# Performance work log

Measured on AMD Instinct MI355X. Metric: run time of the kernel, lower is better.

## Reference

```python
import jax, jax.numpy as jnp
import numpy as np

BINS = 6  # torch.histc(bins=6, min=0, max=256) in rarity()


def _border_mask(h, w, dtype):
    m = jnp.ones((h, w), dtype)
    return m.at[0, :].set(0).at[-1, :].set(0).at[:, 0].set(0).at[:, -1].set(0)


def _norm(x, lo, hi, axes):
    # normalize_tensor: map to [lo,hi]; all-zeros if constant map
    mn = x.min(axes, keepdims=True)
    mx = x.max(axes, keepdims=True)
    d = mx - mn
    ds = jnp.where(d == 0, jnp.ones_like(d), d)
    out = (x - mn) / ds * (hi - lo) + lo
    return jnp.where(d == 0, jnp.zeros_like(out), out)


def _ponder(x, axes):
    # map_ponderation: normalize to [0,1] then scale by (max-mean)^2
    w = (x.max(axes, keepdims=True) - x.mean(axes, keepdims=True)) ** 2
    return _norm(x, 0.0, 1.0, axes) * w


def _rarity_all(ch):
    # Vectorized rarity() over all channels. ch: [C,H,W]
    C, H, W = ch.shape
    ch = ch * _border_mask(H, W, ch.dtype)          # zero 1-px border
    ch = _norm(ch, 0.0, 256.0, (1, 2))              # per-channel -> [0,256]
    # torch.histc over [0,256]: bin = floor(v*bins/256), max value in last bin
    bin_idx = jnp.clip((ch * (BINS / 256.0)).astype(jnp.int32), 0, BINS - 1)
    hist = jax.nn.one_hot(bin_idx, BINS, dtype=ch.dtype).sum((1, 2))  # [C,BINS]
    hist = hist / hist.sum(-1, keepdims=True)
    hist = -jnp.log(hist + 1e-4)
    # lookup: (channel*bins - 1).long().clamp(0, bins-1)  (channel in [0,256], as in source)
    lut_idx = jnp.clip((ch * BINS - 1).astype(jnp.int32), 0, BINS - 1)
    dst = hist[jnp.arange(C)[:, None, None], lut_idx]  # [C,H,W] rarity lookup
    dst = _norm(dst, 0.0, 1.0, (1, 2))
    return _ponder(dst, (1, 2))


def _apply_rarity(x):
    # x: [1,C,H,W] -> [H,W]
    ch = x[0]
    H, W = ch.shape[-2:]
    r = _rarity_all(ch)
    # channel 0: ponderated again, no extra border zeroing (as in source)
    p0 = _ponder(r[0], (0, 1))
    rest = r[1:] * _border_mask(H, W, r.dtype)  # channels 1..C-1: border zeroed
    p = p0 + _ponder(rest, (1, 2)).sum(0)
    return _norm(p, 0.0, 1.0, (0, 1))  # threshold=None -> no thresholding


def _resize240(m):
    # T.Resize((240,240), bilinear) ~ half-pixel linear resize
    return jax.image.resize(m, (240, 240), method='linear')


def _forward(layers):
    # group layers into packs by spatial resolution (static, shapes known)
    packs = {}
    for t in layers:
        packs.setdefault(t.shape[-2:], []).append(t)
    group_maps = []
    for pack in packs.values():
        maps = [_resize240(_apply_rarity(t)) for t in pack]
        fused = maps[0] * 0.0
        for m in maps:  # fuse_itti
            fused = fused + _ponder(m, (0, 1))
        group_maps.append(_norm(fused, 0.0, 256.0, (0, 1)))
    groups = jnp.stack(group_maps, -1)  # [240,240,n_packs]
    return groups.sum(-1), groups


def setup_inputs() -> dict:
    key = jax.random.key(0)
    shapes = ([(1, 64, 224, 224)] * 2 + [(1, 128, 112, 112)] * 2 +
              [(1, 256, 56, 56)] * 3 + [(1, 512, 28, 28)] * 3 +
              [(1, 512, 14, 14)] * 3)
    keys = jax.random.split(key, len(shapes))
    return {f"x{i}": jax.random.uniform(keys[i], s, jnp.float32)
            for i, s in enumerate(shapes)}


def reference(x0, x1, x2, x3, x4, x5, x6, x7, x8, x9, x10, x11, x12):
    return _forward([x0, x1, x2, x3, x4, x5, x6, x7, x8, x9, x10, x11, x12])
```

## Files before the change

kernel.cpp:

```cpp
#include <hip/hip_runtime.h>
#include <math.h>

#define NT 13
#define RHW 57600

typedef unsigned long long ull;

struct Meta {
  const float* x[NT];
  int C[NT];
  int H[NT];
  float hsc[NT];
  int chanOff[NT + 1];
  int pixOff[NT + 1];
  int nibOff[NT];
  int pmOff[NT + 1];
};

__device__ __forceinline__ int segOf(const int* off, int b) {
  int t = 0;
  while (t + 1 < NT && b >= off[t + 1]) t++;
  return t;
}

template <int HH>
__device__ __forceinline__ void mmA(const float* __restrict__ ch, float& mn, float& mx) {
  constexpr int W = HH, H = HH;
  constexpr int f4n = (H * W) / 4;
  for (int i4 = (int)threadIdx.x; i4 < f4n; i4 += 512) {
    float4 v = reinterpret_cast<const float4*>(ch)[i4];
#pragma unroll
    for (int j = 0; j < 4; j++) {
      int idx = i4 * 4 + j;
      int h = idx / W, w = idx - h * W;
      bool ok = h > 0 && h < (H - 1) && w > 0 && w < (W - 1);
      float f = (j == 0) ? v.x : (j == 1) ? v.y : (j == 2) ? v.z : v.w;
      if (ok) { mn = fminf(mn, f); mx = fmaxf(mx, f); }
    }
  }
}

template <int HH>
__device__ __forceinline__ void histB(const float* __restrict__ ch, unsigned short* __restrict__ nb,
                                      float mn, float invd, ull& cbin, ull& clut) {
  constexpr int W = HH, H = HH;
  constexpr int f4n = (H * W) / 4;
  for (int i4 = (int)threadIdx.x; i4 < f4n; i4 += 512) {
    float4 v = reinterpret_cast<const float4*>(ch)[i4];
    unsigned pack = 0;
#pragma unroll
    for (int j = 0; j < 4; j++) {
      int idx = i4 * 4 + j;
      int h = idx / W, w = idx - h * W;
      bool intr = h > 0 && h < (H - 1) && w > 0 && w < (W - 1);
      float f = (j == 0) ? v.x : (j == 1) ? v.y : (j == 2) ? v.z : v.w;
      float vv = (f - mn) * invd * 256.0f;
      int bin = (int)(vv * 0.0234375f);
      bin = bin < 0 ? 0 : (bin > 5 ? 5 : bin);
      float tt = vv * 6.0f - 1.0f;
      int li = (int)tt;
      li = li < 0 ? 0 : (li > 5 ? 5 : li);
      cbin += (ull)intr << (bin * 10);
      clut += (ull)intr << (li * 10);
      pack |= (unsigned)(intr ? li : 7) << (4 * j);
    }
    nb[i4] = (unsigned short)pack;
  }
}

__device__ __forceinline__ void lutMath(int c, int H, int HW, float mn, float invd,
                                        unsigned* hh, float* LUT ) {
  float fHW = (float)HW;
  int nbp = 4 * H - 4;
  float vb = (0.f - mn) * invd * 256.0f;
  int bin_b = (int)(vb * 0.0234375f);
  bin_b = bin_b < 0 ? 0 : (bin_b > 5 ? 5 : bin_b);
  float ttb = vb * 6.0f - 1.0f;
  int lib = (int)ttb;
  lib = lib < 0 ? 0 : (lib > 5 ? 5 : lib);
  hh[bin_b] += (unsigned)nbp;
  hh[6 + lib] += (unsigned)nbp;
  float hl[6];
#pragma unroll
  for (int j = 0; j < 6; j++) hl[j] = -logf((float)hh[j] / fHW + 1e-4f);
  float mn2 = INFINITY, mx2 = -INFINITY, sum2 = 0.f;
#pragma unroll
  for (int j = 0; j < 6; j++) {
    unsigned cc = hh[6 + j];
    if (cc) { mn2 = fminf(mn2, hl[j]); mx2 = fmaxf(mx2, hl[j]); sum2 += (float)cc * hl[j]; }
  }
  float d2 = mx2 - mn2;
  float RL[6];
  if (d2 > 0.f) {
    float meanN = (sum2 / fHW - mn2) / d2;
    float w = 1.0f - meanN; w *= w;
#pragma unroll
    for (int j = 0; j < 6; j++) RL[j] = (hl[j] - mn2) / d2 * w;
  } else {
#pragma unroll
    for (int j = 0; j < 6; j++) RL[j] = 0.f;
  }
  if (c == 0) {
    float mnr = INFINITY, mxr = -INFINITY, sumr = 0.f;
#pragma unroll
    for (int j = 0; j < 6; j++) {
      unsigned cc = hh[6 + j];
      if (cc) { mnr = fminf(mnr, RL[j]); mxr = fmaxf(mxr, RL[j]); sumr += (float)cc * RL[j]; }
    }
    float dr = mxr - mnr;
    if (dr > 0.f) {
      float meanr = sumr / fHW;
      float wp = mxr - meanr; wp *= wp;
#pragma unroll
      for (int j = 0; j < 6; j++) LUT[j] = (RL[j] - mnr) / dr * wp;
      LUT[6] = LUT[lib];
    } else {
#pragma unroll
      for (int j = 0; j < 7; j++) LUT[j] = 0.f;
    }
  } else {
    float mnr = 0.f, mxr = 0.f, sumr = 0.f;
#pragma unroll
    for (int j = 0; j < 6; j++) {
      int cc = (int)hh[6 + j] - (j == lib ? nbp : 0);
      if (cc > 0) { mnr = fminf(mnr, RL[j]); mxr = fmaxf(mxr, RL[j]); sumr += (float)cc * RL[j]; }
    }
    float dr = mxr - mnr;
    if (dr > 0.f) {
      float meanr = sumr / fHW;
      float wp = mxr - meanr; wp *= wp;
#pragma unroll
      for (int j = 0; j < 6; j++) LUT[j] = (RL[j] - mnr) / dr * wp;
      LUT[6] = (0.f - mnr) / dr * wp;
    } else {
#pragma unroll
      for (int j = 0; j < 7; j++) LUT[j] = 0.f;
    }
  }
}

__global__ __launch_bounds__(512) void k_chan(Meta m, unsigned short* __restrict__ nib,
                                              float* __restrict__ lutg) {
  int b = blockIdx.x;
  int t = segOf(m.chanOff, b);
  int c = b - m.chanOff[t];
  int H = m.H[t], HW = H * H;
  const float* ch = m.x[t] + (size_t)c * HW;
  int tid = threadIdx.x, wid = tid >> 6, lane = tid & 63;

  float mn = INFINITY, mx = -INFINITY;
  switch (H) {
    case 224: mmA<224>(ch, mn, mx); break;
    case 112: mmA<112>(ch, mn, mx); break;
    case 56:  mmA<56>(ch, mn, mx); break;
    case 28:  mmA<28>(ch, mn, mx); break;
    default:  mmA<14>(ch, mn, mx); break;
  }
#pragma unroll
  for (int o = 32; o > 0; o >>= 1) {
    mn = fminf(mn, __shfl_down(mn, o));
    mx = fmaxf(mx, __shfl_down(mx, o));
  }
  __shared__ float smn[8], smx[8];
  __shared__ float sMn, sInv;
  if (lane == 0) { smn[wid] = mn; smx[wid] = mx; }
  __syncthreads();
  if (tid == 0) {
    for (int i = 1; i < 8; i++) { mn = fminf(mn, smn[i]); mx = fmaxf(mx, smx[i]); }
    mn = fminf(mn, 0.f); mx = fmaxf(mx, 0.f);
    float d = mx - mn;
    sMn = mn; sInv = d > 0.f ? 1.0f / d : 0.f;
  }
  __syncthreads();
  float mnc = sMn, invd = sInv;

  unsigned short* nb = nib + m.nibOff[t] + (size_t)c * (HW >> 2);
  ull cbin = 0ull, clut = 0ull;
  switch (H) {
    case 224: histB<224>(ch, nb, mnc, invd, cbin, clut); break;
    case 112: histB<112>(ch, nb, mnc, invd, cbin, clut); break;
    case 56:  histB<56>(ch, nb, mnc, invd, cbin, clut); break;
    case 28:  histB<28>(ch, nb, mnc, invd, cbin, clut); break;
    default:  histB<14>(ch, nb, mnc, invd, cbin, clut); break;
  }
  unsigned pk[6];
#pragma unroll
  for (int j = 0; j < 6; j++)
    pk[j] = (unsigned)((cbin >> (10 * j)) & 1023ull) |
            ((unsigned)((clut >> (10 * j)) & 1023ull) << 16);
#pragma unroll
  for (int o = 32; o > 0; o >>= 1) {
#pragma unroll
    for (int j = 0; j < 6; j++) pk[j] += __shfl_down(pk[j], o);
  }
  __shared__ unsigned spk[8][6];
  if (lane == 0) {
#pragma unroll
    for (int j = 0; j < 6; j++) spk[wid][j] = pk[j];
  }
  __syncthreads();
  if (tid == 0) {
    unsigned hh[12];
#pragma unroll
    for (int j = 0; j < 6; j++) {
      unsigned s = 0;
#pragma unroll
      for (int w = 0; w < 8; w++) s += spk[w][j];
      hh[j] = s & 0xffffu; hh[6 + j] = s >> 16;
    }
    float LUT[7];
    lutMath(c, H, HW, mnc, invd, hh, LUT);
    float* o = lutg + (size_t)b * 8;
#pragma unroll
    for (int j = 0; j < 6; j++) o[j] = LUT[j];
    o[6] = LUT[6]; o[7] = LUT[6];
  }
}

__global__ __launch_bounds__(256) void k_pmap(Meta m, const unsigned short* __restrict__ nib,
                                              const float* __restrict__ lutg,
                                              float* __restrict__ pmaps, float* __restrict__ ppart) {
  __shared__ float sLut[512 * 8];
  __shared__ float sAcc[4][256];
  int b = blockIdx.x;
  int t = segOf(m.pmOff, b);
  int blk = b - m.pmOff[t];
  int C = m.C[t], HW = m.H[t] * m.H[t], i4n = HW >> 2;
  int tid = threadIdx.x, wid = tid >> 6, lane = tid & 63;
  const float4* Lg = reinterpret_cast<const float4*>(lutg + (size_t)m.chanOff[t] * 8);
  for (int i = tid; i < C * 2; i += 256) reinterpret_cast<float4*>(sLut)[i] = Lg[i];
  __syncthreads();
  int i4 = blk * 64 + lane;
  bool act = i4 < i4n;
  float a0 = 0.f, a1 = 0.f, a2 = 0.f, a3 = 0.f;
  if (act) {
    const unsigned short* nb = nib + m.nibOff[t] + i4;
    int cpw = C >> 2;
    int c0 = wid * cpw, c1 = c0 + cpw;
#pragma unroll 4
    for (int c = c0; c < c1; ++c) {
      unsigned n = nb[(size_t)c * i4n];
      a0 += sLut[c * 8 + (int)(n & 7u)];
      a1 += sLut[c * 8 + (int)((n >> 4) & 7u)];
      a2 += sLut[c * 8 + (int)((n >> 8) & 7u)];
      a3 += sLut[c * 8 + (int)((n >> 12) & 7u)];
    }
  }
  *reinterpret_cast<float4*>(&sAcc[wid][lane * 4]) = make_float4(a0, a1, a2, a3);
  __syncthreads();
  if (wid == 0) {
    float bmn = INFINITY, bmx = -INFINITY;
    if (act) {
      float t0 = 0.f, t1 = 0.f, t2 = 0.f, t3 = 0.f;
#pragma unroll
      for (int w = 0; w < 4; w++) {
        const float* s = &sAcc[w][lane * 4];
        t0 += s[0]; t1 += s[1]; t2 += s[2]; t3 += s[3];
      }
      *reinterpret_cast<float4*>(pmaps + (size_t)m.pixOff[t] + (size_t)i4 * 4) =
          make_float4(t0, t1, t2, t3);
      bmn = fminf(fminf(t0, t1), fminf(t2, t3));
      bmx = fmaxf(fmaxf(t0, t1), fmaxf(t2, t3));
    }
#pragma unroll
    for (int o = 32; o > 0; o >>= 1) {
      bmn = fminf(bmn, __shfl_down(bmn, o));
      bmx = fmaxf(bmx, __shfl_down(bmx, o));
    }
    if (lane == 0) { ppart[2 * b] = bmn; ppart[2 * b + 1] = bmx; }
  }
}

__global__ __launch_bounds__(256) void k_resize(Meta m, const float* pmaps, const float* ppart,
                                                float* mmaps, float* rpart) {
  __shared__ float sMnT, sInvT;
  int t = blockIdx.x / 225;
  int blk = blockIdx.x % 225;
  int wid = threadIdx.x >> 6, lane = threadIdx.x & 63;
  if (wid == 0) {
    int n = m.pmOff[t + 1] - m.pmOff[t];
    const float* pp = ppart + (size_t)m.pmOff[t] * 2;
    float mn = INFINITY, mx = -INFINITY;
    for (int i = lane; i < n; i += 64) { mn = fminf(mn, pp[2 * i]); mx = fmaxf(mx, pp[2 * i + 1]); }
#pragma unroll
    for (int o = 32; o > 0; o >>= 1) {
      mn = fminf(mn, __shfl_down(mn, o));
      mx = fmaxf(mx, __shfl_down(mx, o));
    }
    if (lane == 0) {
      float d = mx - mn;
      sMnT = mn; sInvT = d > 0.f ? 1.0f / d : 0.f;
    }
  }
  __syncthreads();
  int pix = blk * 256 + threadIdx.x;
  int H = m.H[t], W = m.H[t];
  const float* p = pmaps + m.pixOff[t];
  float mn = sMnT, a = sInvT;
  int oy = pix / 240, ox = pix - oy * 240;
  float hs = m.hsc[t];
  float sy = ((float)oy + 0.5f) * hs - 0.5f;
  float sx = ((float)ox + 0.5f) * hs - 0.5f;
  float fy0 = floorf(sy), fx0 = floorf(sx);
  float fy = sy - fy0, fx = sx - fx0;
  int iy0 = (int)fy0, ix0 = (int)fx0;
  int y0 = iy0 < 0 ? 0 : (iy0 > H - 1 ? H - 1 : iy0);
  int y1 = iy0 + 1 < 0 ? 0 : (iy0 + 1 > H - 1 ? H - 1 : iy0 + 1);
  int x0 = ix0 < 0 ? 0 : (ix0 > W - 1 ? W - 1 : ix0);
  int x1 = ix0 + 1 < 0 ? 0 : (ix0 + 1 > W - 1 ? W - 1 : ix0 + 1);
  float v00 = p[y0 * W + x0], v01 = p[y0 * W + x1];
  float v10 = p[y1 * W + x0], v11 = p[y1 * W + x1];
  float r = (1.f - fy) * ((1.f - fx) * v00 + fx * v01) + fy * ((1.f - fx) * v10 + fx * v11);
  float mv = (r - mn) * a;
  mmaps[(size_t)t * RHW + pix] = mv;
  float bmn = mv, bmx = mv, bsm = mv;
#pragma unroll
  for (int o = 32; o > 0; o >>= 1) {
    bmn = fminf(bmn, __shfl_down(bmn, o));
    bmx = fmaxf(bmx, __shfl_down(bmx, o));
    bsm += __shfl_down(bsm, o);
  }
  __shared__ float smn[4], smx[4], ssm[4];
  if ((threadIdx.x & 63) == 0) { smn[wid] = bmn; smx[wid] = bmx; ssm[wid] = bsm; }
  __syncthreads();
  if (threadIdx.x == 0) {
    for (int i = 1; i < 4; i++) { bmn = fminf(bmn, smn[i]); bmx = fmaxf(bmx, smx[i]); bsm += ssm[i]; }
    float* rp = rpart + ((size_t)t * 225 + blk) * 3;
    rp[0] = bmn; rp[1] = bmx; rp[2] = bsm;
  }
}

__global__ __launch_bounds__(256) void k_fuse(const float* mmaps, const float* rpart,
                                              float* fusedm, float* fpart) {
  __shared__ float sMn[3], sD[3], sW[3];
  int g = blockIdx.x / 225;
  int blk = blockIdx.x % 225;
  const int gs[6] = {0, 2, 4, 7, 10, 13};
  int nt = gs[g + 1] - gs[g];
  int wid = threadIdx.x >> 6, lane = threadIdx.x & 63;
  if (wid < nt) {
    int t = gs[g] + wid;
    const float* rp = rpart + (size_t)t * 225 * 3;
    float mn = INFINITY, mx = -INFINITY, sm = 0.f;
    for (int i = lane; i < 225; i += 64) {
      mn = fminf(mn, rp[3 * i]); mx = fmaxf(mx, rp[3 * i + 1]); sm += rp[3 * i + 2];
    }
#pragma unroll
    for (int o = 32; o > 0; o >>= 1) {
      mn = fminf(mn, __shfl_down(mn, o));
      mx = fmaxf(mx, __shfl_down(mx, o));
      sm += __shfl_down(sm, o);
    }
    if (lane == 0) {
      float d = mx - mn;
      if (d > 0.f) {
        float mean = sm * (1.0f / 57600.0f);
        float w = mx - mean; w *= w;
        sMn[wid] = mn; sD[wid] = d; sW[wid] = w;
      } else {
        sMn[wid] = 0.f; sD[wid] = 0.f; sW[wid] = 0.f;
      }
    }
  }
  __syncthreads();
  int pix = blk * 256 + threadIdx.x;
  float acc = 0.f;
  for (int k = 0; k < nt; k++) {
    int t = gs[g] + k;
    if (sD[k] > 0.f) acc += (mmaps[(size_t)t * RHW + pix] - sMn[k]) / sD[k] * sW[k];
  }
  fusedm[(size_t)g * RHW + pix] = acc;
  float bmn = acc, bmx = acc;
#pragma unroll
  for (int o = 32; o > 0; o >>= 1) {
    bmn = fminf(bmn, __shfl_down(bmn, o));
    bmx = fmaxf(bmx, __shfl_down(bmx, o));
  }
  __shared__ float smn[4], smx[4];
  if ((threadIdx.x & 63) == 0) { smn[wid] = bmn; smx[wid] = bmx; }
  __syncthreads();
  if (threadIdx.x == 0) {
    for (int i = 1; i < 4; i++) { bmn = fminf(bmn, smn[i]); bmx = fmaxf(bmx, smx[i]); }
    float* fp = fpart + ((size_t)g * 225 + blk) * 2;
    fp[0] = bmn; fp[1] = bmx;
  }
}

__global__ __launch_bounds__(256) void k_out(const float* fusedm, const float* fpart, float* out) {
  __shared__ float fmn[5], finv[5];
  int wid = threadIdx.x >> 6, lane = threadIdx.x & 63;
  for (int g = wid; g < 5; g += 4) {
    const float* fp = fpart + (size_t)g * 225 * 2;
    float mn = INFINITY, mx = -INFINITY;
    for (int i = lane; i < 225; i += 64) {
      mn = fminf(mn, fp[2 * i]); mx = fmaxf(mx, fp[2 * i + 1]);
    }
#pragma unroll
    for (int o = 32; o > 0; o >>= 1) {
      mn = fminf(mn, __shfl_down(mn, o));
      mx = fmaxf(mx, __shfl_down(mx, o));
    }
    if (lane == 0) {
      float d = mx - mn;
      fmn[g] = mn; finv[g] = d > 0.f ? 256.0f / d : 0.f;
    }
  }
  __syncthreads();
  int pix = blockIdx.x * 256 + threadIdx.x;
  float acc = 0.f;
  float* out2 = out + RHW;
#pragma unroll
  for (int g = 0; g < 5; g++) {
    float v = (fusedm[(size_t)g * RHW + pix] - fmn[g]) * finv[g];
    out2[(size_t)pix * 5 + g] = v;
    acc += v;
  }
  out[pix] = acc;
}

extern "C" void kernel_launch(void* const* d_in, const int* in_sizes, int n_in,
                              void* d_out, int out_size, void* d_ws, size_t ws_size,
                              hipStream_t stream) {
  static const int Cs[NT] = {64, 64, 128, 128, 256, 256, 256, 512, 512, 512, 512, 512, 512};
  static const int Hs[NT] = {224, 224, 112, 112, 56, 56, 56, 28, 28, 28, 14, 14, 14};
  Meta m;
  int co = 0, po = 0, pmb = 0, nibTot = 0;
  for (int t = 0; t < NT; t++) {
    m.x[t] = (const float*)d_in[t];
    m.C[t] = Cs[t]; m.H[t] = Hs[t];
    m.hsc[t] = (float)((double)Hs[t] / 240.0);
    int HW = Hs[t] * Hs[t];
    m.chanOff[t] = co; co += Cs[t];
    m.pixOff[t] = po; po += HW;
    m.nibOff[t] = nibTot; nibTot += Cs[t] * (HW >> 2);
    m.pmOff[t] = pmb; pmb += (HW + 255) / 256;
  }
  m.chanOff[NT] = co; m.pixOff[NT] = po; m.pmOff[NT] = pmb;

  size_t off = 0;
  auto a16 = [](size_t x) { return (x + 15) & ~(size_t)15; };
#define WALLOC(var, type, count) type* var = (type*)((char*)d_ws + off); off = a16(off + sizeof(type) * (size_t)(count));
  WALLOC(nib, unsigned short, nibTot)
  WALLOC(lutg, float, 8 * co)
  WALLOC(ppart, float, 2 * pmb)
  WALLOC(rpart, float, NT * 225 * 3)
  WALLOC(fpart, float, 5 * 225 * 2)
  WALLOC(pmaps, float, po)
  WALLOC(mmaps, float, NT * RHW)
  WALLOC(fusedm, float, 5 * RHW)
#undef WALLOC

  hipLaunchKernelGGL(k_chan, dim3(co), dim3(512), 0, stream, m, nib, lutg);
  hipLaunchKernelGGL(k_pmap, dim3(pmb), dim3(256), 0, stream, m, nib, lutg, pmaps, ppart);
  hipLaunchKernelGGL(k_resize, dim3(NT * 225), dim3(256), 0, stream, m, pmaps, ppart, mmaps, rpart);
  hipLaunchKernelGGL(k_fuse, dim3(5 * 225), dim3(256), 0, stream, mmaps, rpart, fusedm, fpart);
  hipLaunchKernelGGL(k_out, dim3(225), dim3(256), 0, stream, fusedm, fpart, (float*)d_out);
}
```

Measured before the change: 75.55 us.

## Split per-channel min/max and histogram into chunked kernels, build LUTs in pmap

The single per-channel kernel is replaced by two grid-wide kernels over 8192-pixel chunks: one writes partial min/max, the other reduces those partials, writes the nibble map and writes partial histograms. The aim is to spread the large 224x224 and 112x112 channels across many blocks, so one block per big channel no longer forms a long tail. Each k_pmap block now combines the partials and recomputes every channel's rarity LUT in shared memory, which drops the lutg buffer. The cost is an extra kernel launch, a second read of the input in a separate kernel, and LUT math (including logs) repeated in every pmap block.

```diff
diff --git a/kernel.cpp b/kernel.cpp
--- a/kernel.cpp
+++ b/kernel.cpp
@@ -3,6 +3,7 @@
 
 #define NT 13
 #define RHW 57600
+#define PIXB 8192
 
 typedef unsigned long long ull;
 
@@ -11,9 +12,10 @@
   int C[NT];
   int H[NT];
   float hsc[NT];
-  int chanOff[NT + 1];
   int pixOff[NT + 1];
   int nibOff[NT];
+  int mmOff[NT + 1];
+  int nchMM[NT];
   int pmOff[NT + 1];
 };
 
@@ -24,10 +26,11 @@
 }
 
 template <int HH>
-__device__ __forceinline__ void mmA(const float* __restrict__ ch, float& mn, float& mx) {
+__device__ __forceinline__ void mm_body(const float* __restrict__ ch, int pix0, int pix1,
+                                        float& mn, float& mx) {
   constexpr int W = HH, H = HH;
-  constexpr int f4n = (H * W) / 4;
-  for (int i4 = (int)threadIdx.x; i4 < f4n; i4 += 512) {
+  int i40 = pix0 >> 2, i41 = pix1 >> 2;
+  for (int i4 = i40 + (int)threadIdx.x; i4 < i41; i4 += 256) {
     float4 v = reinterpret_cast<const float4*>(ch)[i4];
 #pragma unroll
     for (int j = 0; j < 4; j++) {
@@ -40,12 +43,46 @@
   }
 }
 
+__global__ __launch_bounds__(256) void k_minmax(Meta m, float* cpart) {
+  int b = blockIdx.x;
+  int t = segOf(m.mmOff, b);
+  int local = b - m.mmOff[t];
+  int nch = m.nchMM[t];
+  int c = local / nch, k = local - c * nch;
+  int HW = m.H[t] * m.H[t];
+  const float* ch = m.x[t] + (size_t)c * HW;
+  int pix0 = k * PIXB, pix1 = min(pix0 + PIXB, HW);
+  float mn = INFINITY, mx = -INFINITY;
+  switch (m.H[t]) {
+    case 224: mm_body<224>(ch, pix0, pix1, mn, mx); break;
+    case 112: mm_body<112>(ch, pix0, pix1, mn, mx); break;
+    case 56:  mm_body<56>(ch, pix0, pix1, mn, mx); break;
+    case 28:  mm_body<28>(ch, pix0, pix1, mn, mx); break;
+    default:  mm_body<14>(ch, pix0, pix1, mn, mx); break;
+  }
+#pragma unroll
+  for (int o = 32; o > 0; o >>= 1) {
+    mn = fminf(mn, __shfl_down(mn, o));
+    mx = fmaxf(mx, __shfl_down(mx, o));
+  }
+  __shared__ float smn[4], smx[4];
+  int wid = threadIdx.x >> 6;
+  if ((threadIdx.x & 63) == 0) { smn[wid] = mn; smx[wid] = mx; }
+  __syncthreads();
+  if (threadIdx.x == 0) {
+    for (int i = 1; i < 4; i++) { mn = fminf(mn, smn[i]); mx = fmaxf(mx, smx[i]); }
+    cpart[2 * b] = mn; cpart[2 * b + 1] = mx;
+  }
+}
+
 template <int HH>
-__device__ __forceinline__ void histB(const float* __restrict__ ch, unsigned short* __restrict__ nb,
-                                      float mn, float invd, ull& cbin, ull& clut) {
+__device__ __forceinline__ void hist_body(const float* __restrict__ ch,
+                                          unsigned short* __restrict__ nb,
+                                          int pix0, int pix1, float mn, float invd,
+                                          ull& cbin, ull& clut) {
   constexpr int W = HH, H = HH;
-  constexpr int f4n = (H * W) / 4;
-  for (int i4 = (int)threadIdx.x; i4 < f4n; i4 += 512) {
+  int i40 = pix0 >> 2, i41 = pix1 >> 2;
+  for (int i4 = i40 + (int)threadIdx.x; i4 < i41; i4 += 256) {
     float4 v = reinterpret_cast<const float4*>(ch)[i4];
     unsigned pack = 0;
 #pragma unroll
@@ -68,8 +105,74 @@
   }
 }
 
-__device__ __forceinline__ void lutMath(int c, int H, int HW, float mn, float invd,
-                                        unsigned* hh, float* LUT ) {
+__global__ __launch_bounds__(256) void k_histnib(Meta m, const float* __restrict__ cpart,
+                                                 unsigned* __restrict__ hpart,
+                                                 unsigned short* __restrict__ nib) {
+  int b = blockIdx.x;
+  int t = segOf(m.mmOff, b);
+  int local = b - m.mmOff[t];
+  int nch = m.nchMM[t];
+  int c = local / nch, k = local - c * nch;
+  int H = m.H[t], HW = H * H;
+  const float* ch = m.x[t] + (size_t)c * HW;
+  int cb = m.mmOff[t] + c * nch;
+  float mn = INFINITY, mx = -INFINITY;
+  for (int kk = 0; kk < nch; kk++) {
+    mn = fminf(mn, cpart[2 * (cb + kk)]);
+    mx = fmaxf(mx, cpart[2 * (cb + kk) + 1]);
+  }
+  mn = fminf(mn, 0.f);
+  mx = fmaxf(mx, 0.f);
+  float d = mx - mn;
+  float invd = d > 0.f ? 1.0f / d : 0.f;
+  unsigned short* nb = nib + m.nibOff[t] + (size_t)c * (HW >> 2);
+  int pix0 = k * PIXB, pix1 = min(pix0 + PIXB, HW);
+  ull cbin = 0ull, clut = 0ull;
+  switch (H) {
+    case 224: hist_body<224>(ch, nb, pix0, pix1, mn, invd, cbin, clut); break;
+    case 112: hist_body<112>(ch, nb, pix0, pix1, mn, invd, cbin, clut); break;
+    case 56:  hist_body<56>(ch, nb, pix0, pix1, mn, invd, cbin, clut); break;
+    case 28:  hist_body<28>(ch, nb, pix0, pix1, mn, invd, cbin, clut); break;
+    default:  hist_body<14>(ch, nb, pix0, pix1, mn, invd, cbin, clut); break;
+  }
+  unsigned pk[6];
+#pragma unroll
+  for (int j = 0; j < 6; j++)
+    pk[j] = (unsigned)((cbin >> (10 * j)) & 1023ull) |
+            ((unsigned)((clut >> (10 * j)) & 1023ull) << 16);
+#pragma unroll
+  for (int o = 32; o > 0; o >>= 1) {
+#pragma unroll
+    for (int j = 0; j < 6; j++) pk[j] += __shfl_down(pk[j], o);
+  }
+  __shared__ unsigned swh[4][12];
+  int wid = threadIdx.x >> 6, lane = threadIdx.x & 63;
+  if (lane == 0) {
+#pragma unroll
+    for (int j = 0; j < 6; j++) { swh[wid][j] = pk[j] & 0xffffu; swh[wid][6 + j] = pk[j] >> 16; }
+  }
+  __syncthreads();
+  if (threadIdx.x < 12)
+    hpart[12 * b + threadIdx.x] =
+        swh[0][threadIdx.x] + swh[1][threadIdx.x] + swh[2][threadIdx.x] + swh[3][threadIdx.x];
+}
+
+__device__ __forceinline__ void buildLut(int c, int H, int HW, int cb, int nch,
+                                         const float* __restrict__ cpart,
+                                         const unsigned* __restrict__ hpart, float* sLut) {
+  float mn = INFINITY, mx = -INFINITY;
+  unsigned hh[12];
+#pragma unroll
+  for (int j = 0; j < 12; j++) hh[j] = 0u;
+  for (int k = 0; k < nch; k++) {
+    mn = fminf(mn, cpart[2 * (cb + k)]);
+    mx = fmaxf(mx, cpart[2 * (cb + k) + 1]);
+#pragma unroll
+    for (int j = 0; j < 12; j++) hh[j] += hpart[12 * (cb + k) + j];
+  }
+  mn = fminf(mn, 0.f); mx = fmaxf(mx, 0.f);
+  float d = mx - mn;
+  float invd = d > 0.f ? 1.0f / d : 0.f;
   float fHW = (float)HW;
   int nbp = 4 * H - 4;
   float vb = (0.f - mn) * invd * 256.0f;
@@ -100,6 +203,7 @@
 #pragma unroll
     for (int j = 0; j < 6; j++) RL[j] = 0.f;
   }
+  float LUT[7];
   if (c == 0) {
     float mnr = INFINITY, mxr = -INFINITY, sumr = 0.f;
 #pragma unroll
@@ -137,98 +241,26 @@
       for (int j = 0; j < 7; j++) LUT[j] = 0.f;
     }
   }
-}
-
-__global__ __launch_bounds__(512) void k_chan(Meta m, unsigned short* __restrict__ nib,
-                                              float* __restrict__ lutg) {
-  int b = blockIdx.x;
-  int t = segOf(m.chanOff, b);
-  int c = b - m.chanOff[t];
-  int H = m.H[t], HW = H * H;
-  const float* ch = m.x[t] + (size_t)c * HW;
-  int tid = threadIdx.x, wid = tid >> 6, lane = tid & 63;
-
-  float mn = INFINITY, mx = -INFINITY;
-  switch (H) {
-    case 224: mmA<224>(ch, mn, mx); break;
-    case 112: mmA<112>(ch, mn, mx); break;
-    case 56:  mmA<56>(ch, mn, mx); break;
-    case 28:  mmA<28>(ch, mn, mx); break;
-    default:  mmA<14>(ch, mn, mx); break;
-  }
-#pragma unroll
-  for (int o = 32; o > 0; o >>= 1) {
-    mn = fminf(mn, __shfl_down(mn, o));
-    mx = fmaxf(mx, __shfl_down(mx, o));
-  }
-  __shared__ float smn[8], smx[8];
-  __shared__ float sMn, sInv;
-  if (lane == 0) { smn[wid] = mn; smx[wid] = mx; }
-  __syncthreads();
-  if (tid == 0) {
-    for (int i = 1; i < 8; i++) { mn = fminf(mn, smn[i]); mx = fmaxf(mx, smx[i]); }
-    mn = fminf(mn, 0.f); mx = fmaxf(mx, 0.f);
-    float d = mx - mn;
-    sMn = mn; sInv = d > 0.f ? 1.0f / d : 0.f;
-  }
-  __syncthreads();
-  float mnc = sMn, invd = sInv;
-
-  unsigned short* nb = nib + m.nibOff[t] + (size_t)c * (HW >> 2);
-  ull cbin = 0ull, clut = 0ull;
-  switch (H) {
-    case 224: histB<224>(ch, nb, mnc, invd, cbin, clut); break;
-    case 112: histB<112>(ch, nb, mnc, invd, cbin, clut); break;
-    case 56:  histB<56>(ch, nb, mnc, invd, cbin, clut); break;
-    case 28:  histB<28>(ch, nb, mnc, invd, cbin, clut); break;
-    default:  histB<14>(ch, nb, mnc, invd, cbin, clut); break;
-  }
-  unsigned pk[6];
-#pragma unroll
-  for (int j = 0; j < 6; j++)
-    pk[j] = (unsigned)((cbin >> (10 * j)) & 1023ull) |
-            ((unsigned)((clut >> (10 * j)) & 1023ull) << 16);
-#pragma unroll
-  for (int o = 32; o > 0; o >>= 1) {
-#pragma unroll
-    for (int j = 0; j < 6; j++) pk[j] += __shfl_down(pk[j], o);
-  }
-  __shared__ unsigned spk[8][6];
-  if (lane == 0) {
-#pragma unroll
-    for (int j = 0; j < 6; j++) spk[wid][j] = pk[j];
-  }
-  __syncthreads();
-  if (tid == 0) {
-    unsigned hh[12];
-#pragma unroll
-    for (int j = 0; j < 6; j++) {
-      unsigned s = 0;
-#pragma unroll
-      for (int w = 0; w < 8; w++) s += spk[w][j];
-      hh[j] = s & 0xffffu; hh[6 + j] = s >> 16;
-    }
-    float LUT[7];
-    lutMath(c, H, HW, mnc, invd, hh, LUT);
-    float* o = lutg + (size_t)b * 8;
-#pragma unroll
-    for (int j = 0; j < 6; j++) o[j] = LUT[j];
-    o[6] = LUT[6]; o[7] = LUT[6];
-  }
-}
-
-__global__ __launch_bounds__(256) void k_pmap(Meta m, const unsigned short* __restrict__ nib,
-                                              const float* __restrict__ lutg,
+#pragma unroll
+  for (int j = 0; j < 6; j++) sLut[c * 8 + j] = LUT[j];
+  sLut[c * 8 + 6] = LUT[6];
+  sLut[c * 8 + 7] = LUT[6];
+}
+
+__global__ __launch_bounds__(256) void k_pmap(Meta m, const float* __restrict__ cpart,
+                                              const unsigned* __restrict__ hpart,
+                                              const unsigned short* __restrict__ nib,
                                               float* __restrict__ pmaps, float* __restrict__ ppart) {
   __shared__ float sLut[512 * 8];
   __shared__ float sAcc[4][256];
   int b = blockIdx.x;
   int t = segOf(m.pmOff, b);
   int blk = b - m.pmOff[t];
-  int C = m.C[t], HW = m.H[t] * m.H[t], i4n = HW >> 2;
+  int C = m.C[t], H = m.H[t], HW = H * H, i4n = HW >> 2;
+  int nch = m.nchMM[t];
   int tid = threadIdx.x, wid = tid >> 6, lane = tid & 63;
-  const float4* Lg = reinterpret_cast<const float4*>(lutg + (size_t)m.chanOff[t] * 8);
-  for (int i = tid; i < C * 2; i += 256) reinterpret_cast<float4*>(sLut)[i] = Lg[i];
+  for (int c = tid; c < C; c += 256)
+    buildLut(c, H, HW, m.mmOff[t] + c * nch, nch, cpart, hpart, sLut);
   __syncthreads();
   int i4 = blk * 64 + lane;
   bool act = i4 < i4n;
@@ -424,24 +456,27 @@
   static const int Cs[NT] = {64, 64, 128, 128, 256, 256, 256, 512, 512, 512, 512, 512, 512};
   static const int Hs[NT] = {224, 224, 112, 112, 56, 56, 56, 28, 28, 28, 14, 14, 14};
   Meta m;
-  int co = 0, po = 0, pmb = 0, nibTot = 0;
+  int po = 0, mmb = 0, pmb = 0, nibTot = 0;
   for (int t = 0; t < NT; t++) {
     m.x[t] = (const float*)d_in[t];
     m.C[t] = Cs[t]; m.H[t] = Hs[t];
     m.hsc[t] = (float)((double)Hs[t] / 240.0);
     int HW = Hs[t] * Hs[t];
-    m.chanOff[t] = co; co += Cs[t];
     m.pixOff[t] = po; po += HW;
     m.nibOff[t] = nibTot; nibTot += Cs[t] * (HW >> 2);
+    m.mmOff[t] = mmb;
+    m.nchMM[t] = (HW + PIXB - 1) / PIXB;
+    mmb += Cs[t] * m.nchMM[t];
     m.pmOff[t] = pmb; pmb += (HW + 255) / 256;
   }
-  m.chanOff[NT] = co; m.pixOff[NT] = po; m.pmOff[NT] = pmb;
+  m.pixOff[NT] = po; m.mmOff[NT] = mmb; m.pmOff[NT] = pmb;
 
   size_t off = 0;
   auto a16 = [](size_t x) { return (x + 15) & ~(size_t)15; };
 #define WALLOC(var, type, count) type* var = (type*)((char*)d_ws + off); off = a16(off + sizeof(type) * (size_t)(count));
+  WALLOC(cpart, float, 2 * mmb)
+  WALLOC(hpart, unsigned, 12 * mmb)
   WALLOC(nib, unsigned short, nibTot)
-  WALLOC(lutg, float, 8 * co)
   WALLOC(ppart, float, 2 * pmb)
   WALLOC(rpart, float, NT * 225 * 3)
   WALLOC(fpart, float, 5 * 225 * 2)
@@ -450,8 +485,9 @@
   WALLOC(fusedm, float, 5 * RHW)
 #undef WALLOC
 
-  hipLaunchKernelGGL(k_chan, dim3(co), dim3(512), 0, stream, m, nib, lutg);
-  hipLaunchKernelGGL(k_pmap, dim3(pmb), dim3(256), 0, stream, m, nib, lutg, pmaps, ppart);
+  hipLaunchKernelGGL(k_minmax, dim3(mmb), dim3(256), 0, stream, m, cpart);
+  hipLaunchKernelGGL(k_histnib, dim3(mmb), dim3(256), 0, stream, m, cpart, hpart, nib);
+  hipLaunchKernelGGL(k_pmap, dim3(pmb), dim3(256), 0, stream, m, cpart, hpart, nib, pmaps, ppart);
   hipLaunchKernelGGL(k_resize, dim3(NT * 225), dim3(256), 0, stream, m, pmaps, ppart, mmaps, rpart);
   hipLaunchKernelGGL(k_fuse, dim3(5 * 225), dim3(256), 0, stream, mmaps, rpart, fusedm, fpart);
   hipLaunchKernelGGL(k_out, dim3(225), dim3(256), 0, stream, fusedm, fpart, (float*)d_out);
```

Result: slower. 78.95 us (+4.5%).
